# Kernel tuning notes

Hardware: AMD Instinct MI355X
Metric: run time of the kernel (lower is better)

The kernel has to match this reference:

```python
import jax, jax.numpy as jnp
import numpy as np

T, N, RNN, EMB, IN, OUT = 20, 65536, 256, 128, 2, 5

def setup_inputs() -> dict:
    key = jax.random.key(0)
    ks = jax.random.split(key, 12)
    s = 0.05
    return {
        "input_data": jax.random.normal(ks[0], (T - 1, N, IN), jnp.float32),
        "hidden_states": jax.random.normal(ks[1], (N, RNN), jnp.float32) * s,
        "cell_states": jax.random.normal(ks[2], (N, RNN), jnp.float32) * s,
        "mask": jax.random.randint(ks[3], (T - 1, N), 0, 2, jnp.int32),
        "W_emb": jax.random.normal(ks[4], (IN, EMB), jnp.float32) * s,
        "b_emb": jax.random.normal(ks[5], (EMB,), jnp.float32) * s,
        "W_ih": jax.random.normal(ks[6], (4 * RNN, EMB), jnp.float32) * s,
        "b_ih": jax.random.normal(ks[7], (4 * RNN,), jnp.float32) * s,
        "W_hh": jax.random.normal(ks[8], (4 * RNN, RNN), jnp.float32) * s,
        "b_hh": jax.random.normal(ks[9], (4 * RNN,), jnp.float32) * s,
        "W_out": jax.random.normal(ks[10], (OUT, RNN), jnp.float32) * s,
        "b_out": jax.random.normal(ks[11], (OUT,), jnp.float32) * s,
    }


def reference(input_data, hidden_states, cell_states, mask,
              W_emb, b_emb, W_ih, b_ih, W_hh, b_hh, W_out, b_out):
    # Dense masked formulation of the per-frame gather->LSTMCell->scatter loop:
    # inactive nodes keep their states; their outputs stay zero. Dropout p=0 / eval.
    maskb = (mask == 1)  # [T-1, N]

    def step(carry, inp):
        h, c = carry
        x, m = inp                                   # x: [N, IN], m: [N] bool
        e = jax.nn.relu(x @ W_emb + b_emb)           # [N, EMB]
        gates = e @ W_ih.T + b_ih + h @ W_hh.T + b_hh  # [N, 4*RNN]
        i, f, g, o = jnp.split(gates, 4, axis=-1)    # PyTorch LSTMCell gate order
        i = jax.nn.sigmoid(i)
        f = jax.nn.sigmoid(f)
        g = jnp.tanh(g)
        o = jax.nn.sigmoid(o)
        c_new = f * c + i * g
        h_new = o * jnp.tanh(c_new)
        out = h_new @ W_out.T + b_out                # [N, OUT]
        mm = m[:, None]
        h = jnp.where(mm, h_new, h)
        c = jnp.where(mm, c_new, c)
        out = jnp.where(mm, out, jnp.zeros_like(out))
        return (h, c), out

    (h_final, c_final), outputs = jax.lax.scan(step, (hidden_states, cell_states),
                                               (input_data, maskb))
    return outputs, h_final, c_final
```

## Files before the change

kernel.cpp:

```cpp
#include <hip/hip_runtime.h>

#define T_STEPS 19
#define NBATCH  65536
#define RNN     256
#define EMB     128
#define KDIM    384
#define ROWB    768
#define SWZ(row) (((row) & 15) << 4)

typedef __bf16 bf16x8 __attribute__((ext_vector_type(8)));
typedef float  f32x4  __attribute__((ext_vector_type(4)));

#define BLOCK_SYNC() asm volatile("s_waitcnt lgkmcnt(0)\n\ts_barrier" ::: "memory")

__device__ __forceinline__ unsigned short f2bf(float f) {
    unsigned u = __float_as_uint(f);
    u += 0x7fffu + ((u >> 16) & 1u);
    return (unsigned short)(u >> 16);
}
__device__ __forceinline__ float bf2f(unsigned short u) {
    return __uint_as_float(((unsigned)u) << 16);
}
__device__ __forceinline__ float sigm_(float x) {
    float e = __expf(-x);
    return __builtin_amdgcn_rcpf(1.0f + e);
}
__device__ __forceinline__ float tanh_(float x) {
    float e = __expf(2.0f * x);
    return 1.0f - 2.0f * __builtin_amdgcn_rcpf(e + 1.0f);
}

__global__ void prep_wcat(const float* __restrict__ Whh, const float* __restrict__ Wih,
                          unsigned short* __restrict__ dst) {
    int tid = blockIdx.x * 256 + threadIdx.x;
    int l   = tid & 63;
    int p   = tid >> 6;
    int g   = p & 3;
    int kkw = p >> 2;
    int kk  = kkw % 12;
    int w   = kkw / 12;
    int j   = g * 256 + w * 16 + (l & 15);
    int kb  = kk * 32 + (l >> 4) * 8;
    unsigned short v[8];
#pragma unroll
    for (int e = 0; e < 8; ++e) {
        int k = kb + e;
        float f = (k < 256) ? Whh[j * 256 + k] : Wih[j * 128 + (k - 256)];
        v[e] = f2bf(f);
    }
    uint4 pk;
    pk.x = (unsigned)v[0] | ((unsigned)v[1] << 16);
    pk.y = (unsigned)v[2] | ((unsigned)v[3] << 16);
    pk.z = (unsigned)v[4] | ((unsigned)v[5] << 16);
    pk.w = (unsigned)v[6] | ((unsigned)v[7] << 16);
    ((uint4*)dst)[tid] = pk;
}

__global__ void prep_wout(const float* __restrict__ Wout, unsigned short* __restrict__ dst) {
    int tid = blockIdx.x * 256 + threadIdx.x;
    if (tid >= 512) return;
    int l  = tid & 63;
    int kk = tid >> 6;
    int q  = l & 15;
    int kb = kk * 32 + (l >> 4) * 8;
    unsigned short v[8];
#pragma unroll
    for (int e = 0; e < 8; ++e) {
        float f = (q < 5) ? Wout[q * 256 + kb + e] : 0.0f;
        v[e] = f2bf(f);
    }
    uint4 pk;
    pk.x = (unsigned)v[0] | ((unsigned)v[1] << 16);
    pk.y = (unsigned)v[2] | ((unsigned)v[3] << 16);
    pk.z = (unsigned)v[4] | ((unsigned)v[5] << 16);
    pk.w = (unsigned)v[6] | ((unsigned)v[7] << 16);
    ((uint4*)dst)[tid] = pk;
}

__global__ void prep_bias(const float* __restrict__ bih, const float* __restrict__ bhh,
                          float* __restrict__ dst) {
    int tid = blockIdx.x * 256 + threadIdx.x;
    if (tid < 1024) dst[tid] = bih[tid] + bhh[tid];
}

__global__ __launch_bounds__(1024, 4)
void lstm_main(const float* __restrict__ x_in, const float* __restrict__ h_in,
               const float* __restrict__ c_in, const int* __restrict__ mask,
               const float* __restrict__ W_emb, const float* __restrict__ b_emb,
               const float* __restrict__ b_out,
               const unsigned short* __restrict__ wcat_fr,
               const unsigned short* __restrict__ wout_fr,
               const float* __restrict__ bias_g,
               float* __restrict__ out) {
    __shared__ unsigned short A_lds[64 * KDIM];
    __shared__ float c_lds[64 * RNN];
    __shared__ float we_lds[384];
    __shared__ int   m_lds[2][64];

    const int tid  = threadIdx.x;
    const int lane = tid & 63;
    const int w    = tid >> 6;
    const int base = blockIdx.x * 64;
    const int csub = lane & 15;
    const int kq   = lane >> 2 >> 2;
    const int unit = w * 16 + csub;

#pragma unroll
    for (int m = 0; m < 4; ++m)
#pragma unroll
        for (int r = 0; r < 4; ++r) {
            int row = m * 16 + kq * 4 + r;
            float hv = h_in[(size_t)(base + row) * RNN + unit];
            c_lds[row * RNN + unit] = c_in[(size_t)(base + row) * RNN + unit];
            int byte = row * ROWB + unit * 2;
            byte ^= SWZ(row);
            A_lds[byte >> 1] = f2bf(hv);
        }
    if (tid < 384) we_lds[tid] = (tid < 256) ? W_emb[tid] : b_emb[tid - 256];

    float bias4[4];
#pragma unroll
    for (int g = 0; g < 4; ++g) bias4[g] = bias_g[g * 256 + unit];
    const float bo = (csub < 5) ? b_out[csub] : 0.0f;

    const uint4* wfp = (const uint4*)wcat_fr + (size_t)w * (12 * 4 * 64) + lane;
    const uint4* wop = (const uint4*)wout_fr + lane;

    bf16x8 bA[4], bB[4];
#pragma unroll
    for (int g = 0; g < 4; ++g) bA[g] = *(const bf16x8*)(wfp + (0 * 4 + g) * 64);
#pragma unroll
    for (int g = 0; g < 4; ++g) bB[g] = *(const bf16x8*)(wfp + (1 * 4 + g) * 64);

    BLOCK_SYNC();

    for (int t = 0; t < T_STEPS; ++t) {
        {
            int row = tid >> 4;
            int jc  = (tid & 15) * 8;
            const float* xp = x_in + ((size_t)t * NBATCH + base + row) * 2;
            float x0 = xp[0], x1 = xp[1];
            unsigned pk[4];
#pragma unroll
            for (int e = 0; e < 8; e += 2) {
                int j = jc + e;
                float e0 = fmaxf(fmaf(x0, we_lds[j],     fmaf(x1, we_lds[128 + j],     we_lds[256 + j])),     0.0f);
                float e1 = fmaxf(fmaf(x0, we_lds[j + 1], fmaf(x1, we_lds[128 + j + 1], we_lds[256 + j + 1])), 0.0f);
                pk[e >> 1] = (unsigned)f2bf(e0) | ((unsigned)f2bf(e1) << 16);
            }
            int byte = row * ROWB + 512 + 2 * jc;
            byte ^= SWZ(row);
            *(uint4*)((char*)A_lds + byte) = make_uint4(pk[0], pk[1], pk[2], pk[3]);
            if (tid < 64) m_lds[t & 1][tid] = mask[(size_t)t * NBATCH + base + tid];
        }
        BLOCK_SYNC();

        f32x4 acc[4][4];
#pragma unroll
        for (int m = 0; m < 4; ++m)
#pragma unroll
            for (int g = 0; g < 4; ++g) {
                f32x4 z = {bias4[g], bias4[g], bias4[g], bias4[g]};
                acc[m][g] = z;
            }
#pragma unroll 1
        for (int kp = 0; kp < 6; ++kp) {
            int kk0 = kp * 2;
            {
#pragma unroll
                for (int m = 0; m < 4; ++m) {
                    int row = m * 16 + csub;
                    int byte = row * ROWB + kk0 * 64 + kq * 16;
                    byte ^= SWZ(row);
                    bf16x8 a = *(const bf16x8*)((const char*)A_lds + byte);
                    acc[m][0] = __builtin_amdgcn_mfma_f32_16x16x32_bf16(a, bA[0], acc[m][0], 0, 0, 0);
                    acc[m][1] = __builtin_amdgcn_mfma_f32_16x16x32_bf16(a, bA[1], acc[m][1], 0, 0, 0);
                    acc[m][2] = __builtin_amdgcn_mfma_f32_16x16x32_bf16(a, bA[2], acc[m][2], 0, 0, 0);
                    acc[m][3] = __builtin_amdgcn_mfma_f32_16x16x32_bf16(a, bA[3], acc[m][3], 0, 0, 0);
                }
                int kn = kk0 + 2; if (kn >= 12) kn -= 12;
#pragma unroll
                for (int g = 0; g < 4; ++g)
                    bA[g] = *(const bf16x8*)(wfp + (kn * 4 + g) * 64);
            }
            {
                int kk1 = kk0 + 1;
#pragma unroll
                for (int m = 0; m < 4; ++m) {
                    int row = m * 16 + csub;
                    int byte = row * ROWB + kk1 * 64 + kq * 16;
                    byte ^= SWZ(row);
                    bf16x8 a = *(const bf16x8*)((const char*)A_lds + byte);
                    acc[m][0] = __builtin_amdgcn_mfma_f32_16x16x32_bf16(a, bB[0], acc[m][0], 0, 0, 0);
                    acc[m][1] = __builtin_amdgcn_mfma_f32_16x16x32_bf16(a, bB[1], acc[m][1], 0, 0, 0);
                    acc[m][2] = __builtin_amdgcn_mfma_f32_16x16x32_bf16(a, bB[2], acc[m][2], 0, 0, 0);
                    acc[m][3] = __builtin_amdgcn_mfma_f32_16x16x32_bf16(a, bB[3], acc[m][3], 0, 0, 0);
                }
                int kn = kk1 + 2; if (kn >= 12) kn -= 12;
#pragma unroll
                for (int g = 0; g < 4; ++g)
                    bB[g] = *(const bf16x8*)(wfp + (kn * 4 + g) * 64);
            }
        }
        BLOCK_SYNC();

#pragma unroll
        for (int m = 0; m < 4; ++m)
#pragma unroll
            for (int r = 0; r < 4; ++r) {
                int row = m * 16 + kq * 4 + r;
                float cv = c_lds[row * RNN + unit];
                float iv = sigm_(acc[m][0][r]);
                float fv = sigm_(acc[m][1][r]);
                float gv = tanh_(acc[m][2][r]);
                float ov = sigm_(acc[m][3][r]);
                float cn = fmaf(fv, cv, iv * gv);
                float hn = ov * tanh_(cn);
                if (m_lds[t & 1][row]) {
                    c_lds[row * RNN + unit] = cn;
                    int byte = row * ROWB + unit * 2;
                    byte ^= SWZ(row);
                    A_lds[byte >> 1] = f2bf(hn);
                }
            }
        BLOCK_SYNC();

        if (w < 4) {
            f32x4 oacc = {bo, bo, bo, bo};
#pragma unroll
            for (int kk = 0; kk < 8; ++kk) {
                int row = w * 16 + csub;
                int byte = row * ROWB + kk * 64 + kq * 16;
                byte ^= SWZ(row);
                bf16x8 a  = *(const bf16x8*)((const char*)A_lds + byte);
                bf16x8 bw = *(const bf16x8*)(wop + kk * 64);
                oacc = __builtin_amdgcn_mfma_f32_16x16x32_bf16(a, bw, oacc, 0, 0, 0);
            }
            if (csub < 5) {
#pragma unroll
                for (int r = 0; r < 4; ++r) {
                    int row = w * 16 + kq * 4 + r;
                    int m = m_lds[t & 1][row];
                    out[((size_t)t * NBATCH + base + row) * 5 + csub] = m ? oacc[r] : 0.0f;
                }
            }
        }
    }

    float* hout = out + (size_t)T_STEPS * NBATCH * 5;
    float* cout = hout + (size_t)NBATCH * RNN;
#pragma unroll
    for (int m = 0; m < 4; ++m)
#pragma unroll
        for (int r = 0; r < 4; ++r) {
            int row = m * 16 + kq * 4 + r;
            int byte = row * ROWB + unit * 2;
            byte ^= SWZ(row);
            hout[(size_t)(base + row) * RNN + unit] = bf2f(A_lds[byte >> 1]);
            cout[(size_t)(base + row) * RNN + unit] = c_lds[row * RNN + unit];
        }
}

extern "C" void kernel_launch(void* const* d_in, const int* in_sizes, int n_in,
                              void* d_out, int out_size, void* d_ws, size_t ws_size,
                              hipStream_t stream) {
    (void)in_sizes; (void)n_in; (void)out_size; (void)ws_size;
    const float* x_in = (const float*)d_in[0];
    const float* h0   = (const float*)d_in[1];
    const float* c0   = (const float*)d_in[2];
    const int*   mk   = (const int*)d_in[3];
    const float* Wemb = (const float*)d_in[4];
    const float* bemb = (const float*)d_in[5];
    const float* Wih  = (const float*)d_in[6];
    const float* bih  = (const float*)d_in[7];
    const float* Whh  = (const float*)d_in[8];
    const float* bhh  = (const float*)d_in[9];
    const float* Wout = (const float*)d_in[10];
    const float* bout = (const float*)d_in[11];

    unsigned short* wcat = (unsigned short*)d_ws;
    unsigned short* wouf = wcat + 393216;
    float*          bsg  = (float*)(wouf + 4096);

    prep_wcat<<<192, 256, 0, stream>>>(Whh, Wih, wcat);
    prep_wout<<<2, 256, 0, stream>>>(Wout, wouf);
    prep_bias<<<4, 256, 0, stream>>>(bih, bhh, bsg);

    float* outp = (float*)d_out;
    lstm_main<<<1024, 1024, 0, stream>>>(x_in, h0, c0, mk, Wemb, bemb, bout,
                                         wcat, wouf, bsg, outp);
}
```

Measured before the change: 1.796 ms.

## Double-buffer LDS activation tile to cut per-step barriers in LSTM loop

Replaces the single LDS activation tile with two ping-pong buffers, so each step reads h and the embedding from the current buffer and writes the new h and next-step embedding into the other. This drops two of the three block-wide barriers per timestep. The mask is now loaded per wave and turned into a ballot bitmask instead of being staged through LDS. The embedding for step t+1 is computed in the gate epilogue, with its inputs loaded early, reading W_emb straight from global memory. The cost is LDS usage growing to about the full 160 KB per CU, plus an extra old-h read and copy for masked rows.

```diff
diff --git a/kernel.cpp b/kernel.cpp
--- a/kernel.cpp
+++ b/kernel.cpp
@@ -6,6 +6,7 @@
 #define EMB     128
 #define KDIM    384
 #define ROWB    768
+#define ABUF    49152
 #define SWZ(row) (((row) & 15) << 4)
 
 typedef __bf16 bf16x8 __attribute__((ext_vector_type(8)));
@@ -92,17 +93,15 @@
                const unsigned short* __restrict__ wout_fr,
                const float* __restrict__ bias_g,
                float* __restrict__ out) {
-    __shared__ unsigned short A_lds[64 * KDIM];
+    __shared__ unsigned short A2[2 * 64 * KDIM];
     __shared__ float c_lds[64 * RNN];
-    __shared__ float we_lds[384];
-    __shared__ int   m_lds[2][64];
 
     const int tid  = threadIdx.x;
     const int lane = tid & 63;
     const int w    = tid >> 6;
     const int base = blockIdx.x * 64;
     const int csub = lane & 15;
-    const int kq   = lane >> 2 >> 2;
+    const int kq   = lane >> 4;
     const int unit = w * 16 + csub;
 
 #pragma unroll
@@ -114,9 +113,25 @@
             c_lds[row * RNN + unit] = c_in[(size_t)(base + row) * RNN + unit];
             int byte = row * ROWB + unit * 2;
             byte ^= SWZ(row);
-            A_lds[byte >> 1] = f2bf(hv);
-        }
-    if (tid < 384) we_lds[tid] = (tid < 256) ? W_emb[tid] : b_emb[tid - 256];
+            *(unsigned short*)((char*)A2 + byte) = f2bf(hv);
+        }
+    {
+        int row = tid >> 4;
+        int jc  = (tid & 15) * 8;
+        const float* xp = x_in + ((size_t)(base + row)) * 2;
+        float x0 = xp[0], x1 = xp[1];
+        unsigned pk[4];
+#pragma unroll
+        for (int e = 0; e < 8; e += 2) {
+            int j = jc + e;
+            float e0 = fmaxf(fmaf(x0, W_emb[j],     fmaf(x1, W_emb[128 + j],     b_emb[j])),     0.0f);
+            float e1 = fmaxf(fmaf(x0, W_emb[j + 1], fmaf(x1, W_emb[128 + j + 1], b_emb[j + 1])), 0.0f);
+            pk[e >> 1] = (unsigned)f2bf(e0) | ((unsigned)f2bf(e1) << 16);
+        }
+        int byte = row * ROWB + 512 + 2 * jc;
+        byte ^= SWZ(row);
+        *(uint4*)((char*)A2 + byte) = make_uint4(pk[0], pk[1], pk[2], pk[3]);
+    }
 
     float bias4[4];
 #pragma unroll
@@ -135,25 +150,11 @@
     BLOCK_SYNC();
 
     for (int t = 0; t < T_STEPS; ++t) {
-        {
-            int row = tid >> 4;
-            int jc  = (tid & 15) * 8;
-            const float* xp = x_in + ((size_t)t * NBATCH + base + row) * 2;
-            float x0 = xp[0], x1 = xp[1];
-            unsigned pk[4];
-#pragma unroll
-            for (int e = 0; e < 8; e += 2) {
-                int j = jc + e;
-                float e0 = fmaxf(fmaf(x0, we_lds[j],     fmaf(x1, we_lds[128 + j],     we_lds[256 + j])),     0.0f);
-                float e1 = fmaxf(fmaf(x0, we_lds[j + 1], fmaf(x1, we_lds[128 + j + 1], we_lds[256 + j + 1])), 0.0f);
-                pk[e >> 1] = (unsigned)f2bf(e0) | ((unsigned)f2bf(e1) << 16);
-            }
-            int byte = row * ROWB + 512 + 2 * jc;
-            byte ^= SWZ(row);
-            *(uint4*)((char*)A_lds + byte) = make_uint4(pk[0], pk[1], pk[2], pk[3]);
-            if (tid < 64) m_lds[t & 1][tid] = mask[(size_t)t * NBATCH + base + tid];
-        }
-        BLOCK_SYNC();
+        const int abC = (t & 1) * ABUF;
+        const int abN = ((t + 1) & 1) * ABUF;
+
+        int mv = mask[(size_t)t * NBATCH + base + lane];
+        unsigned long long mbits = __ballot(mv != 0);
 
         f32x4 acc[4][4];
 #pragma unroll
@@ -172,7 +173,7 @@
                     int row = m * 16 + csub;
                     int byte = row * ROWB + kk0 * 64 + kq * 16;
                     byte ^= SWZ(row);
-                    bf16x8 a = *(const bf16x8*)((const char*)A_lds + byte);
+                    bf16x8 a = *(const bf16x8*)((const char*)A2 + abC + byte);
                     acc[m][0] = __builtin_amdgcn_mfma_f32_16x16x32_bf16(a, bA[0], acc[m][0], 0, 0, 0);
                     acc[m][1] = __builtin_amdgcn_mfma_f32_16x16x32_bf16(a, bA[1], acc[m][1], 0, 0, 0);
                     acc[m][2] = __builtin_amdgcn_mfma_f32_16x16x32_bf16(a, bA[2], acc[m][2], 0, 0, 0);
@@ -190,7 +191,7 @@
                     int row = m * 16 + csub;
                     int byte = row * ROWB + kk1 * 64 + kq * 16;
                     byte ^= SWZ(row);
-                    bf16x8 a = *(const bf16x8*)((const char*)A_lds + byte);
+                    bf16x8 a = *(const bf16x8*)((const char*)A2 + abC + byte);
                     acc[m][0] = __builtin_amdgcn_mfma_f32_16x16x32_bf16(a, bB[0], acc[m][0], 0, 0, 0);
                     acc[m][1] = __builtin_amdgcn_mfma_f32_16x16x32_bf16(a, bB[1], acc[m][1], 0, 0, 0);
                     acc[m][2] = __builtin_amdgcn_mfma_f32_16x16x32_bf16(a, bB[2], acc[m][2], 0, 0, 0);
@@ -202,7 +203,13 @@
                     bB[g] = *(const bf16x8*)(wfp + (kn * 4 + g) * 64);
             }
         }
-        BLOCK_SYNC();
+
+        float ex0 = 0.0f, ex1 = 0.0f;
+        int erow = tid >> 4, ejc = (tid & 15) * 8;
+        if (t + 1 < T_STEPS) {
+            const float* xp = x_in + ((size_t)(t + 1) * NBATCH + base + erow) * 2;
+            ex0 = xp[0]; ex1 = xp[1];
+        }
 
 #pragma unroll
         for (int m = 0; m < 4; ++m)
@@ -216,13 +223,29 @@
                 float ov = sigm_(acc[m][3][r]);
                 float cn = fmaf(fv, cv, iv * gv);
                 float hn = ov * tanh_(cn);
-                if (m_lds[t & 1][row]) {
-                    c_lds[row * RNN + unit] = cn;
-                    int byte = row * ROWB + unit * 2;
-                    byte ^= SWZ(row);
-                    A_lds[byte >> 1] = f2bf(hn);
-                }
-            }
+                int msk = (int)((mbits >> row) & 1ull);
+                int hb = row * ROWB + unit * 2;
+                hb ^= SWZ(row);
+                unsigned short hold = *(const unsigned short*)((const char*)A2 + abC + hb);
+                unsigned short hnew = msk ? f2bf(hn) : hold;
+                *(unsigned short*)((char*)A2 + abN + hb) = hnew;
+                if (msk) c_lds[row * RNN + unit] = cn;
+            }
+
+        if (t + 1 < T_STEPS) {
+            unsigned pk[4];
+#pragma unroll
+            for (int e = 0; e < 8; e += 2) {
+                int j = ejc + e;
+                float e0 = fmaxf(fmaf(ex0, W_emb[j],     fmaf(ex1, W_emb[128 + j],     b_emb[j])),     0.0f);
+                float e1 = fmaxf(fmaf(ex0, W_emb[j + 1], fmaf(ex1, W_emb[128 + j + 1], b_emb[j + 1])), 0.0f);
+                pk[e >> 1] = (unsigned)f2bf(e0) | ((unsigned)f2bf(e1) << 16);
+            }
+            int byte = erow * ROWB + 512 + 2 * ejc;
+            byte ^= SWZ(erow);
+            *(uint4*)((char*)A2 + abN + byte) = make_uint4(pk[0], pk[1], pk[2], pk[3]);
+        }
+
         BLOCK_SYNC();
 
         if (w < 4) {
@@ -232,7 +255,7 @@
                 int row = w * 16 + csub;
                 int byte = row * ROWB + kk * 64 + kq * 16;
                 byte ^= SWZ(row);
-                bf16x8 a  = *(const bf16x8*)((const char*)A_lds + byte);
+                bf16x8 a  = *(const bf16x8*)((const char*)A2 + abN + byte);
                 bf16x8 bw = *(const bf16x8*)(wop + kk * 64);
                 oacc = __builtin_amdgcn_mfma_f32_16x16x32_bf16(a, bw, oacc, 0, 0, 0);
             }
@@ -240,13 +263,14 @@
 #pragma unroll
                 for (int r = 0; r < 4; ++r) {
                     int row = w * 16 + kq * 4 + r;
-                    int m = m_lds[t & 1][row];
-                    out[((size_t)t * NBATCH + base + row) * 5 + csub] = m ? oacc[r] : 0.0f;
+                    int msk = (int)((mbits >> row) & 1ull);
+                    out[((size_t)t * NBATCH + base + row) * 5 + csub] = msk ? oacc[r] : 0.0f;
                 }
             }
         }
     }
 
+    const int abF = (T_STEPS & 1) * ABUF;
     float* hout = out + (size_t)T_STEPS * NBATCH * 5;
     float* cout = hout + (size_t)NBATCH * RNN;
 #pragma unroll
@@ -256,7 +280,8 @@
             int row = m * 16 + kq * 4 + r;
             int byte = row * ROWB + unit * 2;
             byte ^= SWZ(row);
-            hout[(size_t)(base + row) * RNN + unit] = bf2f(A_lds[byte >> 1]);
+            hout[(size_t)(base + row) * RNN + unit] =
+                bf2f(*(const unsigned short*)((const char*)A2 + abF + byte));
             cout[(size_t)(base + row) * RNN + unit] = c_lds[row * RNN + unit];
         }
 }
```

Measured after the change: 2.526 ms. 1.41x slower.

## Retile LSTM GEMM so warps split rows and units, keep cell state in registers

Applied to the files above, without the earlier changes.

The work split changes from 16 warps each covering all 64 rows for 16 units to a 4x4 grid: each warp handles 16 rows and 64 units (four 16-unit subtiles across four gates). Weight fragments are reordered to match and streamed from global or L2 each k step with no register double-buffering. Cell state moves from LDS into registers, and biases go to LDS. The aim is fewer A-fragment LDS reads and freed LDS, at the cost of more B-fragment global loads per warp (16 per k step instead of 4) and the loss of the prefetch pipelining.

```diff
diff --git a/kernel.cpp b/kernel.cpp
--- a/kernel.cpp
+++ b/kernel.cpp
@@ -33,14 +33,14 @@
 __global__ void prep_wcat(const float* __restrict__ Whh, const float* __restrict__ Wih,
                           unsigned short* __restrict__ dst) {
     int tid = blockIdx.x * 256 + threadIdx.x;
-    int l   = tid & 63;
-    int p   = tid >> 6;
-    int g   = p & 3;
-    int kkw = p >> 2;
-    int kk  = kkw % 12;
-    int w   = kkw / 12;
-    int j   = g * 256 + w * 16 + (l & 15);
-    int kb  = kk * 32 + (l >> 4) * 8;
+    int l    = tid & 63;
+    int p    = tid >> 6;
+    int usub = p & 3;
+    int g    = (p >> 2) & 3;
+    int kk   = (p >> 4) % 12;
+    int ub   = (p >> 4) / 12;
+    int j    = g * 256 + ub * 64 + usub * 16 + (l & 15);
+    int kb   = kk * 32 + (l >> 4) * 8;
     unsigned short v[8];
 #pragma unroll
     for (int e = 0; e < 8; ++e) {
@@ -93,44 +93,39 @@
                const float* __restrict__ bias_g,
                float* __restrict__ out) {
     __shared__ unsigned short A_lds[64 * KDIM];
-    __shared__ float c_lds[64 * RNN];
+    __shared__ float b_lds[1024];
     __shared__ float we_lds[384];
     __shared__ int   m_lds[2][64];
 
     const int tid  = threadIdx.x;
     const int lane = tid & 63;
     const int w    = tid >> 6;
+    const int ub   = w & 3;
+    const int rb   = w >> 2;
     const int base = blockIdx.x * 64;
     const int csub = lane & 15;
-    const int kq   = lane >> 2 >> 2;
-    const int unit = w * 16 + csub;
-
-#pragma unroll
-    for (int m = 0; m < 4; ++m)
+    const int kq   = lane >> 4;
+
+    float c_reg[4][4];
+
+#pragma unroll
+    for (int usub = 0; usub < 4; ++usub)
 #pragma unroll
         for (int r = 0; r < 4; ++r) {
-            int row = m * 16 + kq * 4 + r;
+            int row  = rb * 16 + kq * 4 + r;
+            int unit = ub * 64 + usub * 16 + csub;
             float hv = h_in[(size_t)(base + row) * RNN + unit];
-            c_lds[row * RNN + unit] = c_in[(size_t)(base + row) * RNN + unit];
+            c_reg[usub][r] = c_in[(size_t)(base + row) * RNN + unit];
             int byte = row * ROWB + unit * 2;
             byte ^= SWZ(row);
             A_lds[byte >> 1] = f2bf(hv);
         }
     if (tid < 384) we_lds[tid] = (tid < 256) ? W_emb[tid] : b_emb[tid - 256];
-
-    float bias4[4];
-#pragma unroll
-    for (int g = 0; g < 4; ++g) bias4[g] = bias_g[g * 256 + unit];
+    if (tid < 1024 && tid >= 0) b_lds[tid] = bias_g[tid];
     const float bo = (csub < 5) ? b_out[csub] : 0.0f;
 
-    const uint4* wfp = (const uint4*)wcat_fr + (size_t)w * (12 * 4 * 64) + lane;
+    const uint4* wfp = (const uint4*)wcat_fr + (size_t)ub * (12 * 16 * 64) + lane;
     const uint4* wop = (const uint4*)wout_fr + lane;
-
-    bf16x8 bA[4], bB[4];
-#pragma unroll
-    for (int g = 0; g < 4; ++g) bA[g] = *(const bf16x8*)(wfp + (0 * 4 + g) * 64);
-#pragma unroll
-    for (int g = 0; g < 4; ++g) bB[g] = *(const bf16x8*)(wfp + (1 * 4 + g) * 64);
 
     BLOCK_SYNC();
 
@@ -157,67 +152,43 @@
 
         f32x4 acc[4][4];
 #pragma unroll
-        for (int m = 0; m < 4; ++m)
-#pragma unroll
-            for (int g = 0; g < 4; ++g) {
-                f32x4 z = {bias4[g], bias4[g], bias4[g], bias4[g]};
-                acc[m][g] = z;
-            }
-#pragma unroll 1
-        for (int kp = 0; kp < 6; ++kp) {
-            int kk0 = kp * 2;
-            {
-#pragma unroll
-                for (int m = 0; m < 4; ++m) {
-                    int row = m * 16 + csub;
-                    int byte = row * ROWB + kk0 * 64 + kq * 16;
-                    byte ^= SWZ(row);
-                    bf16x8 a = *(const bf16x8*)((const char*)A_lds + byte);
-                    acc[m][0] = __builtin_amdgcn_mfma_f32_16x16x32_bf16(a, bA[0], acc[m][0], 0, 0, 0);
-                    acc[m][1] = __builtin_amdgcn_mfma_f32_16x16x32_bf16(a, bA[1], acc[m][1], 0, 0, 0);
-                    acc[m][2] = __builtin_amdgcn_mfma_f32_16x16x32_bf16(a, bA[2], acc[m][2], 0, 0, 0);
-                    acc[m][3] = __builtin_amdgcn_mfma_f32_16x16x32_bf16(a, bA[3], acc[m][3], 0, 0, 0);
-                }
-                int kn = kk0 + 2; if (kn >= 12) kn -= 12;
-#pragma unroll
-                for (int g = 0; g < 4; ++g)
-                    bA[g] = *(const bf16x8*)(wfp + (kn * 4 + g) * 64);
-            }
-            {
-                int kk1 = kk0 + 1;
-#pragma unroll
-                for (int m = 0; m < 4; ++m) {
-                    int row = m * 16 + csub;
-                    int byte = row * ROWB + kk1 * 64 + kq * 16;
-                    byte ^= SWZ(row);
-                    bf16x8 a = *(const bf16x8*)((const char*)A_lds + byte);
-                    acc[m][0] = __builtin_amdgcn_mfma_f32_16x16x32_bf16(a, bB[0], acc[m][0], 0, 0, 0);
-                    acc[m][1] = __builtin_amdgcn_mfma_f32_16x16x32_bf16(a, bB[1], acc[m][1], 0, 0, 0);
-                    acc[m][2] = __builtin_amdgcn_mfma_f32_16x16x32_bf16(a, bB[2], acc[m][2], 0, 0, 0);
-                    acc[m][3] = __builtin_amdgcn_mfma_f32_16x16x32_bf16(a, bB[3], acc[m][3], 0, 0, 0);
-                }
-                int kn = kk1 + 2; if (kn >= 12) kn -= 12;
-#pragma unroll
-                for (int g = 0; g < 4; ++g)
-                    bB[g] = *(const bf16x8*)(wfp + (kn * 4 + g) * 64);
+        for (int g = 0; g < 4; ++g)
+#pragma unroll
+            for (int usub = 0; usub < 4; ++usub) {
+                float b = b_lds[g * 256 + ub * 64 + usub * 16 + csub];
+                f32x4 z = {b, b, b, b};
+                acc[g][usub] = z;
+            }
+#pragma unroll 2
+        for (int kk = 0; kk < 12; ++kk) {
+            int row = rb * 16 + csub;
+            int byte = row * ROWB + kk * 64 + kq * 16;
+            byte ^= SWZ(row);
+            bf16x8 a = *(const bf16x8*)((const char*)A_lds + byte);
+            const uint4* wk = wfp + (size_t)kk * (16 * 64);
+#pragma unroll
+            for (int f = 0; f < 16; ++f) {
+                bf16x8 bfr = *(const bf16x8*)(wk + f * 64);
+                acc[f >> 2][f & 3] =
+                    __builtin_amdgcn_mfma_f32_16x16x32_bf16(a, bfr, acc[f >> 2][f & 3], 0, 0, 0);
             }
         }
         BLOCK_SYNC();
 
 #pragma unroll
-        for (int m = 0; m < 4; ++m)
+        for (int usub = 0; usub < 4; ++usub)
 #pragma unroll
             for (int r = 0; r < 4; ++r) {
-                int row = m * 16 + kq * 4 + r;
-                float cv = c_lds[row * RNN + unit];
-                float iv = sigm_(acc[m][0][r]);
-                float fv = sigm_(acc[m][1][r]);
-                float gv = tanh_(acc[m][2][r]);
-                float ov = sigm_(acc[m][3][r]);
-                float cn = fmaf(fv, cv, iv * gv);
+                int row  = rb * 16 + kq * 4 + r;
+                int unit = ub * 64 + usub * 16 + csub;
+                float iv = sigm_(acc[0][usub][r]);
+                float fv = sigm_(acc[1][usub][r]);
+                float gv = tanh_(acc[2][usub][r]);
+                float ov = sigm_(acc[3][usub][r]);
+                float cn = fmaf(fv, c_reg[usub][r], iv * gv);
                 float hn = ov * tanh_(cn);
                 if (m_lds[t & 1][row]) {
-                    c_lds[row * RNN + unit] = cn;
+                    c_reg[usub][r] = cn;
                     int byte = row * ROWB + unit * 2;
                     byte ^= SWZ(row);
                     A_lds[byte >> 1] = f2bf(hn);
@@ -250,14 +221,15 @@
     float* hout = out + (size_t)T_STEPS * NBATCH * 5;
     float* cout = hout + (size_t)NBATCH * RNN;
 #pragma unroll
-    for (int m = 0; m < 4; ++m)
+    for (int usub = 0; usub < 4; ++usub)
 #pragma unroll
         for (int r = 0; r < 4; ++r) {
-            int row = m * 16 + kq * 4 + r;
+            int row  = rb * 16 + kq * 4 + r;
+            int unit = ub * 64 + usub * 16 + csub;
             int byte = row * ROWB + unit * 2;
             byte ^= SWZ(row);
             hout[(size_t)(base + row) * RNN + unit] = bf2f(A_lds[byte >> 1]);
-            cout[(size_t)(base + row) * RNN + unit] = c_lds[row * RNN + unit];
+            cout[(size_t)(base + row) * RNN + unit] = c_reg[usub][r];
         }
 }
 
```

After: 2.494 ms. 1.39x slower.

## Retile LSTM kernel to 32-row blocks with 512 threads and two unit sub-tiles per wave

Applied to the files above, without the earlier changes.

Halves the batch rows per block to 32 and the block to 8 waves. Each wave now covers 32 hidden units (two 16-wide sub-tiles) over two 16-row M tiles, and the weight fragment layout is reordered to match. Gate biases are staged in LDS, and the embedding weights are read straight from global memory instead of LDS. The smaller LDS footprint and block size are meant to allow more resident blocks per CU and better latency hiding, at the cost of streaming the full weight matrix twice as often per batch row.

```diff
diff --git a/kernel.cpp b/kernel.cpp
--- a/kernel.cpp
+++ b/kernel.cpp
@@ -5,6 +5,7 @@
 #define RNN     256
 #define EMB     128
 #define KDIM    384
+#define ROWS    32
 #define ROWB    768
 #define SWZ(row) (((row) & 15) << 4)
 
@@ -33,14 +34,15 @@
 __global__ void prep_wcat(const float* __restrict__ Whh, const float* __restrict__ Wih,
                           unsigned short* __restrict__ dst) {
     int tid = blockIdx.x * 256 + threadIdx.x;
-    int l   = tid & 63;
-    int p   = tid >> 6;
-    int g   = p & 3;
-    int kkw = p >> 2;
-    int kk  = kkw % 12;
-    int w   = kkw / 12;
-    int j   = g * 256 + w * 16 + (l & 15);
-    int kb  = kk * 32 + (l >> 4) * 8;
+    int l    = tid & 63;
+    int p    = tid >> 6;
+    int g    = p & 3;
+    int usub = (p >> 2) & 1;
+    int kkw  = p >> 3;
+    int kk   = kkw % 12;
+    int w    = kkw / 12;
+    int j    = g * 256 + w * 32 + usub * 16 + (l & 15);
+    int kb   = kk * 32 + (l >> 4) * 8;
     unsigned short v[8];
 #pragma unroll
     for (int e = 0; e < 8; ++e) {
@@ -83,7 +85,7 @@
     if (tid < 1024) dst[tid] = bih[tid] + bhh[tid];
 }
 
-__global__ __launch_bounds__(1024, 4)
+__global__ __launch_bounds__(512, 4)
 void lstm_main(const float* __restrict__ x_in, const float* __restrict__ h_in,
                const float* __restrict__ c_in, const int* __restrict__ mask,
                const float* __restrict__ W_emb, const float* __restrict__ b_emb,
@@ -92,38 +94,36 @@
                const unsigned short* __restrict__ wout_fr,
                const float* __restrict__ bias_g,
                float* __restrict__ out) {
-    __shared__ unsigned short A_lds[64 * KDIM];
-    __shared__ float c_lds[64 * RNN];
-    __shared__ float we_lds[384];
-    __shared__ int   m_lds[2][64];
+    __shared__ unsigned short A_lds[ROWS * KDIM];
+    __shared__ float c_lds[ROWS * RNN];
+    __shared__ float b_lds[1024];
+    __shared__ int   m_lds[2][ROWS];
 
     const int tid  = threadIdx.x;
     const int lane = tid & 63;
     const int w    = tid >> 6;
-    const int base = blockIdx.x * 64;
+    const int base = blockIdx.x * ROWS;
     const int csub = lane & 15;
-    const int kq   = lane >> 2 >> 2;
-    const int unit = w * 16 + csub;
-
-#pragma unroll
-    for (int m = 0; m < 4; ++m)
-#pragma unroll
-        for (int r = 0; r < 4; ++r) {
-            int row = m * 16 + kq * 4 + r;
-            float hv = h_in[(size_t)(base + row) * RNN + unit];
-            c_lds[row * RNN + unit] = c_in[(size_t)(base + row) * RNN + unit];
-            int byte = row * ROWB + unit * 2;
-            byte ^= SWZ(row);
-            A_lds[byte >> 1] = f2bf(hv);
-        }
-    if (tid < 384) we_lds[tid] = (tid < 256) ? W_emb[tid] : b_emb[tid - 256];
-
-    float bias4[4];
-#pragma unroll
-    for (int g = 0; g < 4; ++g) bias4[g] = bias_g[g * 256 + unit];
+    const int kq   = lane >> 4;
+
+#pragma unroll
+    for (int m = 0; m < 2; ++m)
+#pragma unroll
+        for (int usub = 0; usub < 2; ++usub)
+#pragma unroll
+            for (int r = 0; r < 4; ++r) {
+                int row  = m * 16 + kq * 4 + r;
+                int unit = w * 32 + usub * 16 + csub;
+                float hv = h_in[(size_t)(base + row) * RNN + unit];
+                c_lds[row * RNN + unit] = c_in[(size_t)(base + row) * RNN + unit];
+                int byte = (row * ROWB + unit * 2) ^ SWZ(row);
+                A_lds[byte >> 1] = f2bf(hv);
+            }
+    b_lds[tid]       = bias_g[tid];
+    b_lds[tid + 512] = bias_g[tid + 512];
     const float bo = (csub < 5) ? b_out[csub] : 0.0f;
 
-    const uint4* wfp = (const uint4*)wcat_fr + (size_t)w * (12 * 4 * 64) + lane;
+    const uint4* wfp = (const uint4*)wcat_fr + (size_t)w * (12 * 8 * 64) + lane;
     const uint4* wop = (const uint4*)wout_fr + lane;
 
     bf16x8 bA[4], bB[4];
@@ -144,94 +144,94 @@
 #pragma unroll
             for (int e = 0; e < 8; e += 2) {
                 int j = jc + e;
-                float e0 = fmaxf(fmaf(x0, we_lds[j],     fmaf(x1, we_lds[128 + j],     we_lds[256 + j])),     0.0f);
-                float e1 = fmaxf(fmaf(x0, we_lds[j + 1], fmaf(x1, we_lds[128 + j + 1], we_lds[256 + j + 1])), 0.0f);
+                float e0 = fmaxf(fmaf(x0, W_emb[j],     fmaf(x1, W_emb[128 + j],     b_emb[j])),     0.0f);
+                float e1 = fmaxf(fmaf(x0, W_emb[j + 1], fmaf(x1, W_emb[128 + j + 1], b_emb[j + 1])), 0.0f);
                 pk[e >> 1] = (unsigned)f2bf(e0) | ((unsigned)f2bf(e1) << 16);
             }
-            int byte = row * ROWB + 512 + 2 * jc;
-            byte ^= SWZ(row);
+            int byte = (row * ROWB + 512 + 2 * jc) ^ SWZ(row);
             *(uint4*)((char*)A_lds + byte) = make_uint4(pk[0], pk[1], pk[2], pk[3]);
-            if (tid < 64) m_lds[t & 1][tid] = mask[(size_t)t * NBATCH + base + tid];
+            if (tid < ROWS) m_lds[t & 1][tid] = mask[(size_t)t * NBATCH + base + tid];
         }
         BLOCK_SYNC();
 
-        f32x4 acc[4][4];
-#pragma unroll
-        for (int m = 0; m < 4; ++m)
-#pragma unroll
-            for (int g = 0; g < 4; ++g) {
-                f32x4 z = {bias4[g], bias4[g], bias4[g], bias4[g]};
-                acc[m][g] = z;
-            }
+        f32x4 acc[2][2][4];
+#pragma unroll
+        for (int m = 0; m < 2; ++m)
+#pragma unroll
+            for (int usub = 0; usub < 2; ++usub)
+#pragma unroll
+                for (int g = 0; g < 4; ++g) {
+                    float b = b_lds[g * 256 + w * 32 + usub * 16 + csub];
+                    f32x4 z = {b, b, b, b};
+                    acc[m][usub][g] = z;
+                }
 #pragma unroll 1
-        for (int kp = 0; kp < 6; ++kp) {
-            int kk0 = kp * 2;
+        for (int hp = 0; hp < 12; ++hp) {
+            int b0 = (csub * ROWB + hp * 64 + kq * 16) ^ SWZ(csub);
+            bf16x8 a0 = *(const bf16x8*)((const char*)A_lds + b0);
+            int row1 = 16 + csub;
+            int b1 = (row1 * ROWB + hp * 64 + kq * 16) ^ SWZ(row1);
+            bf16x8 a1 = *(const bf16x8*)((const char*)A_lds + b1);
             {
-#pragma unroll
-                for (int m = 0; m < 4; ++m) {
-                    int row = m * 16 + csub;
-                    int byte = row * ROWB + kk0 * 64 + kq * 16;
-                    byte ^= SWZ(row);
-                    bf16x8 a = *(const bf16x8*)((const char*)A_lds + byte);
-                    acc[m][0] = __builtin_amdgcn_mfma_f32_16x16x32_bf16(a, bA[0], acc[m][0], 0, 0, 0);
-                    acc[m][1] = __builtin_amdgcn_mfma_f32_16x16x32_bf16(a, bA[1], acc[m][1], 0, 0, 0);
-                    acc[m][2] = __builtin_amdgcn_mfma_f32_16x16x32_bf16(a, bA[2], acc[m][2], 0, 0, 0);
-                    acc[m][3] = __builtin_amdgcn_mfma_f32_16x16x32_bf16(a, bA[3], acc[m][3], 0, 0, 0);
-                }
-                int kn = kk0 + 2; if (kn >= 12) kn -= 12;
+                acc[0][0][0] = __builtin_amdgcn_mfma_f32_16x16x32_bf16(a0, bA[0], acc[0][0][0], 0, 0, 0);
+                acc[1][0][0] = __builtin_amdgcn_mfma_f32_16x16x32_bf16(a1, bA[0], acc[1][0][0], 0, 0, 0);
+                acc[0][0][1] = __builtin_amdgcn_mfma_f32_16x16x32_bf16(a0, bA[1], acc[0][0][1], 0, 0, 0);
+                acc[1][0][1] = __builtin_amdgcn_mfma_f32_16x16x32_bf16(a1, bA[1], acc[1][0][1], 0, 0, 0);
+                acc[0][0][2] = __builtin_amdgcn_mfma_f32_16x16x32_bf16(a0, bA[2], acc[0][0][2], 0, 0, 0);
+                acc[1][0][2] = __builtin_amdgcn_mfma_f32_16x16x32_bf16(a1, bA[2], acc[1][0][2], 0, 0, 0);
+                acc[0][0][3] = __builtin_amdgcn_mfma_f32_16x16x32_bf16(a0, bA[3], acc[0][0][3], 0, 0, 0);
+                acc[1][0][3] = __builtin_amdgcn_mfma_f32_16x16x32_bf16(a1, bA[3], acc[1][0][3], 0, 0, 0);
+                int hn = 2 * hp + 2; if (hn >= 24) hn -= 24;
 #pragma unroll
                 for (int g = 0; g < 4; ++g)
-                    bA[g] = *(const bf16x8*)(wfp + (kn * 4 + g) * 64);
+                    bA[g] = *(const bf16x8*)(wfp + (hn * 4 + g) * 64);
             }
             {
-                int kk1 = kk0 + 1;
-#pragma unroll
-                for (int m = 0; m < 4; ++m) {
-                    int row = m * 16 + csub;
-                    int byte = row * ROWB + kk1 * 64 + kq * 16;
-                    byte ^= SWZ(row);
-                    bf16x8 a = *(const bf16x8*)((const char*)A_lds + byte);
-                    acc[m][0] = __builtin_amdgcn_mfma_f32_16x16x32_bf16(a, bB[0], acc[m][0], 0, 0, 0);
-                    acc[m][1] = __builtin_amdgcn_mfma_f32_16x16x32_bf16(a, bB[1], acc[m][1], 0, 0, 0);
-                    acc[m][2] = __builtin_amdgcn_mfma_f32_16x16x32_bf16(a, bB[2], acc[m][2], 0, 0, 0);
-                    acc[m][3] = __builtin_amdgcn_mfma_f32_16x16x32_bf16(a, bB[3], acc[m][3], 0, 0, 0);
-                }
-                int kn = kk1 + 2; if (kn >= 12) kn -= 12;
+                acc[0][1][0] = __builtin_amdgcn_mfma_f32_16x16x32_bf16(a0, bB[0], acc[0][1][0], 0, 0, 0);
+                acc[1][1][0] = __builtin_amdgcn_mfma_f32_16x16x32_bf16(a1, bB[0], acc[1][1][0], 0, 0, 0);
+                acc[0][1][1] = __builtin_amdgcn_mfma_f32_16x16x32_bf16(a0, bB[1], acc[0][1][1], 0, 0, 0);
+                acc[1][1][1] = __builtin_amdgcn_mfma_f32_16x16x32_bf16(a1, bB[1], acc[1][1][1], 0, 0, 0);
+                acc[0][1][2] = __builtin_amdgcn_mfma_f32_16x16x32_bf16(a0, bB[2], acc[0][1][2], 0, 0, 0);
+                acc[1][1][2] = __builtin_amdgcn_mfma_f32_16x16x32_bf16(a1, bB[2], acc[1][1][2], 0, 0, 0);
+                acc[0][1][3] = __builtin_amdgcn_mfma_f32_16x16x32_bf16(a0, bB[3], acc[0][1][3], 0, 0, 0);
+                acc[1][1][3] = __builtin_amdgcn_mfma_f32_16x16x32_bf16(a1, bB[3], acc[1][1][3], 0, 0, 0);
+                int hn = 2 * hp + 3; if (hn >= 24) hn -= 24;
 #pragma unroll
                 for (int g = 0; g < 4; ++g)
-                    bB[g] = *(const bf16x8*)(wfp + (kn * 4 + g) * 64);
+                    bB[g] = *(const bf16x8*)(wfp + (hn * 4 + g) * 64);
             }
         }
         BLOCK_SYNC();
 
 #pragma unroll
-        for (int m = 0; m < 4; ++m)
-#pragma unroll
-            for (int r = 0; r < 4; ++r) {
-                int row = m * 16 + kq * 4 + r;
-                float cv = c_lds[row * RNN + unit];
-                float iv = sigm_(acc[m][0][r]);
-                float fv = sigm_(acc[m][1][r]);
-                float gv = tanh_(acc[m][2][r]);
-                float ov = sigm_(acc[m][3][r]);
-                float cn = fmaf(fv, cv, iv * gv);
-                float hn = ov * tanh_(cn);
-                if (m_lds[t & 1][row]) {
-                    c_lds[row * RNN + unit] = cn;
-                    int byte = row * ROWB + unit * 2;
-                    byte ^= SWZ(row);
-                    A_lds[byte >> 1] = f2bf(hn);
+        for (int m = 0; m < 2; ++m)
+#pragma unroll
+            for (int usub = 0; usub < 2; ++usub)
+#pragma unroll
+                for (int r = 0; r < 4; ++r) {
+                    int row  = m * 16 + kq * 4 + r;
+                    int unit = w * 32 + usub * 16 + csub;
+                    float cv = c_lds[row * RNN + unit];
+                    float iv = sigm_(acc[m][usub][0][r]);
+                    float fv = sigm_(acc[m][usub][1][r]);
+                    float gv = tanh_(acc[m][usub][2][r]);
+                    float ov = sigm_(acc[m][usub][3][r]);
+                    float cn = fmaf(fv, cv, iv * gv);
+                    float hn = ov * tanh_(cn);
+                    if (m_lds[t & 1][row]) {
+                        c_lds[row * RNN + unit] = cn;
+                        int byte = (row * ROWB + unit * 2) ^ SWZ(row);
+                        A_lds[byte >> 1] = f2bf(hn);
+                    }
                 }
-            }
         BLOCK_SYNC();
 
-        if (w < 4) {
+        if (w < 2) {
             f32x4 oacc = {bo, bo, bo, bo};
 #pragma unroll
             for (int kk = 0; kk < 8; ++kk) {
                 int row = w * 16 + csub;
-                int byte = row * ROWB + kk * 64 + kq * 16;
-                byte ^= SWZ(row);
+                int byte = (row * ROWB + kk * 64 + kq * 16) ^ SWZ(row);
                 bf16x8 a  = *(const bf16x8*)((const char*)A_lds + byte);
                 bf16x8 bw = *(const bf16x8*)(wop + kk * 64);
                 oacc = __builtin_amdgcn_mfma_f32_16x16x32_bf16(a, bw, oacc, 0, 0, 0);
@@ -240,8 +240,8 @@
 #pragma unroll
                 for (int r = 0; r < 4; ++r) {
                     int row = w * 16 + kq * 4 + r;
-                    int m = m_lds[t & 1][row];
-                    out[((size_t)t * NBATCH + base + row) * 5 + csub] = m ? oacc[r] : 0.0f;
+                    int msk = m_lds[t & 1][row];
+                    out[((size_t)t * NBATCH + base + row) * 5 + csub] = msk ? oacc[r] : 0.0f;
                 }
             }
         }
@@ -250,15 +250,17 @@
     float* hout = out + (size_t)T_STEPS * NBATCH * 5;
     float* cout = hout + (size_t)NBATCH * RNN;
 #pragma unroll
-    for (int m = 0; m < 4; ++m)
-#pragma unroll
-        for (int r = 0; r < 4; ++r) {
-            int row = m * 16 + kq * 4 + r;
-            int byte = row * ROWB + unit * 2;
-            byte ^= SWZ(row);
-            hout[(size_t)(base + row) * RNN + unit] = bf2f(A_lds[byte >> 1]);
-            cout[(size_t)(base + row) * RNN + unit] = c_lds[row * RNN + unit];
-        }
+    for (int m = 0; m < 2; ++m)
+#pragma unroll
+        for (int usub = 0; usub < 2; ++usub)
+#pragma unroll
+            for (int r = 0; r < 4; ++r) {
+                int row  = m * 16 + kq * 4 + r;
+                int unit = w * 32 + usub * 16 + csub;
+                int byte = (row * ROWB + unit * 2) ^ SWZ(row);
+                hout[(size_t)(base + row) * RNN + unit] = bf2f(A_lds[byte >> 1]);
+                cout[(size_t)(base + row) * RNN + unit] = c_lds[row * RNN + unit];
+            }
 }
 
 extern "C" void kernel_launch(void* const* d_in, const int* in_sizes, int n_in,
@@ -287,6 +289,6 @@
     prep_bias<<<4, 256, 0, stream>>>(bih, bhh, bsg);
 
     float* outp = (float*)d_out;
-    lstm_main<<<1024, 1024, 0, stream>>>(x_in, h0, c0, mk, Wemb, bemb, bout,
-                                         wcat, wouf, bsg, outp);
-}
+    lstm_main<<<2048, 512, 0, stream>>>(x_in, h0, c0, mk, Wemb, bemb, bout,
+                                        wcat, wouf, bsg, outp);
+}
```

Measured after the change: 2.108 ms. 17.3% more time.
